# Optimization experiments

Hardware: AMD Instinct MI355X
Metric: run time of the kernel (lower is better)

The kernel has to match this reference:

```python
import jax, jax.numpy as jnp
import numpy as np

START_ID = 1  # id of the start symbol in the vocabulary


def setup_inputs() -> dict:
    key = jax.random.key(0)
    ks = jax.random.split(key, 11)
    B, T, V, E, H, F = 64, 32, 10000, 300, 256, 4096
    s = 0.05
    return {
        "X": jax.random.normal(ks[0], (B, F), jnp.float32),
        "emb_table": jax.random.normal(ks[1], (V, E), jnp.float32),
        "fc1_w": jax.random.normal(ks[2], (H, F), jnp.float32) * s,
        "fc1_b": jax.random.normal(ks[3], (H,), jnp.float32) * s,
        "w_ih": jax.random.normal(ks[4], (4 * H, H + E), jnp.float32) * s,
        "w_hh": jax.random.normal(ks[5], (4 * H, H), jnp.float32) * s,
        "b_ih": jax.random.normal(ks[6], (4 * H,), jnp.float32) * s,
        "b_hh": jax.random.normal(ks[7], (4 * H,), jnp.float32) * s,
        "fc2_w": jax.random.normal(ks[8], (V, H), jnp.float32) * s,
        "fc2_b": jax.random.normal(ks[9], (V,), jnp.float32) * s,
        "label": jax.random.randint(ks[10], (T, B), 0, V, jnp.int64),
        "max_sentence_len": T,
    }


def reference(X, emb_table, fc1_w, fc1_b, w_ih, w_hh, b_ih, b_hh, fc2_w, fc2_b,
              label, max_sentence_len):
    T = max_sentence_len
    B = X.shape[0]
    V, H = fc2_w.shape
    E = emb_table.shape[1]

    # fc1: project image features to hidden size
    Xp = X @ fc1_w.T + fc1_b  # [B, H]

    # word embedding input per step: step 1 uses start symbol,
    # step idx>=2 uses teacher-forced embedding of label[idx-1]
    start_emb = jnp.broadcast_to(emb_table[START_ID], (1, B, E))
    tf_emb = emb_table[label[1:T - 1]]          # [T-2, B, E]
    embeds = jnp.concatenate([start_emb, tf_emb], axis=0)  # [T-1, B, E]

    h0 = jnp.zeros((B, H), X.dtype)
    c0 = jnp.zeros((B, H), X.dtype)

    def step(carry, e):
        h, c = carry
        x = jnp.concatenate([Xp, e], axis=1)  # [B, H+E]
        gates = x @ w_ih.T + b_ih + h @ w_hh.T + b_hh  # [B, 4H]
        i, f, g, o = jnp.split(gates, 4, axis=1)
        i = jax.nn.sigmoid(i)
        f = jax.nn.sigmoid(f)
        g = jnp.tanh(g)
        o = jax.nn.sigmoid(o)
        c = f * c + i * g
        h = o * jnp.tanh(c)
        logp = jax.nn.log_softmax(h @ fc2_w.T + fc2_b, axis=-1)  # [B, V]
        return (h, c), logp

    _, probs = jax.lax.scan(step, (h0, c0), embeds)  # [T-1, B, V]

    # first timestep: one-hot of the start word (as in the torch code)
    start_onehot = jnp.zeros((1, B, V), X.dtype).at[:, :, START_ID].set(1.0)
    result = jnp.concatenate([start_onehot, probs], axis=0)  # [T, B, V]
    return jnp.transpose(result, (1, 0, 2))  # [B, T, V]
```

## Files before the change

kernel.cpp:

```cpp
#include <hip/hip_runtime.h>
#include <hip/hip_bf16.h>
#include <math.h>

#define B_   64
#define T_   32
#define S_   31
#define V_   10000
#define E_   300
#define H_   256
#define F_   4096
#define G4   1024
#define HE   556
#define MPAD 2048
#define NPAD 10112
#define START_ID 1
#define NBL  4

typedef __bf16 bf16x8 __attribute__((ext_vector_type(8)));
typedef float  f32x4  __attribute__((ext_vector_type(4)));

__device__ __forceinline__ float bf16bits_to_f(unsigned int u) {
    union { unsigned int i; float f; } c; c.i = u; return c.f;
}
__device__ __forceinline__ unsigned short f_to_bf16bits(float f) {
    union { float f; unsigned int i; } c; c.f = f;
    unsigned int r = c.i + 0x7fffu + ((c.i >> 16) & 1);
    return (unsigned short)(r >> 16);
}
__device__ __forceinline__ float sigm(float x) { return 1.f / (1.f + __expf(-x)); }
__device__ __forceinline__ float tanh_fast(float x) { return 1.f - 2.f / (__expf(2.f * x) + 1.f); }

__global__ void k_prep(const float* __restrict__ fc2_w,
                       __hip_bfloat16* __restrict__ fc2bf,
                       __hip_bfloat16* __restrict__ Hs,
                       float* __restrict__ Xp) {
    size_t i = (size_t)blockIdx.x * 256 + threadIdx.x;
    float v = (i < (size_t)V_ * H_) ? fc2_w[i] : 0.f;
    fc2bf[i] = __float2bfloat16(v);
    if (i < (size_t)(MPAD - S_ * B_) * H_)
        Hs[(size_t)S_ * B_ * H_ + i] = __float2bfloat16(0.f);
    if (i < B_ * H_) Xp[i] = 0.f;
}

__global__ void k_wpack(const float* __restrict__ w_hh, unsigned short* __restrict__ wpack) {
    int tid = blockIdx.x * 256 + threadIdx.x;
    int lane = tid & 63, frag = tid >> 6;
    int kf = frag & 7, nt = (frag >> 3) & 7, w = frag >> 6;
    int l16 = lane & 15, quad = lane >> 4;
    int j = (l16 & 3) * 256 + w * 32 + nt * 4 + (l16 >> 2);
    int k0 = kf * 32 + quad * 8;
    const float* src = w_hh + (size_t)j * H_ + k0;
    float4 a0 = *(const float4*)(src);
    float4 a1 = *(const float4*)(src + 4);
    unsigned short pk[8];
    pk[0] = f_to_bf16bits(a0.x); pk[1] = f_to_bf16bits(a0.y);
    pk[2] = f_to_bf16bits(a0.z); pk[3] = f_to_bf16bits(a0.w);
    pk[4] = f_to_bf16bits(a1.x); pk[5] = f_to_bf16bits(a1.y);
    pk[6] = f_to_bf16bits(a1.z); pk[7] = f_to_bf16bits(a1.w);
    uint4 st;
    st.x = (unsigned)pk[0] | ((unsigned)pk[1] << 16);
    st.y = (unsigned)pk[2] | ((unsigned)pk[3] << 16);
    st.z = (unsigned)pk[4] | ((unsigned)pk[5] << 16);
    st.w = (unsigned)pk[6] | ((unsigned)pk[7] << 16);
    *(uint4*)(wpack + (size_t)frag * 512 + lane * 8) = st;
}

__global__ void k_onehot(float* __restrict__ out) {
    int i = blockIdx.x * 256 + threadIdx.x;
    if (i < B_ * V_) {
        int b = i / V_, v = i - b * V_;
        out[(size_t)b * T_ * V_ + v] = (v == START_ID) ? 1.f : 0.f;
    }
}

__global__ void k_xp(const float* __restrict__ X, const float* __restrict__ fc1_w,
                     const float* __restrict__ fc1_b, float* __restrict__ Xp) {
    __shared__ __align__(16) float xs[1024];
    int b = blockIdx.x, q = blockIdx.y;
    const float4* xrow = (const float4*)(X + (size_t)b * F_ + q * 1024);
    if (threadIdx.x < 256) ((float4*)xs)[threadIdx.x] = xrow[threadIdx.x];
    __syncthreads();
    int k = threadIdx.x;
    const float4* w = (const float4*)(fc1_w + (size_t)k * F_ + q * 1024);
    float acc = 0.f;
    #pragma unroll 8
    for (int f = 0; f < 256; ++f) {
        float4 wv = w[f];
        float4 xv = ((const float4*)xs)[f];
        acc += wv.x * xv.x + wv.y * xv.y + wv.z * xv.z + wv.w * xv.w;
    }
    if (q == 0) acc += fc1_b[k];
    atomicAdd(&Xp[b * H_ + k], acc);
}

__global__ void k_gconst(const float* __restrict__ Xp, const float* __restrict__ w_ih,
                         const float* __restrict__ b_ih, const float* __restrict__ b_hh,
                         float* __restrict__ gconst) {
    __shared__ __align__(16) float xs[H_];
    int b = blockIdx.x;
    xs[threadIdx.x] = Xp[b * H_ + threadIdx.x];
    __syncthreads();
    #pragma unroll
    for (int q = 0; q < 4; ++q) {
        int j = threadIdx.x + q * 256;
        const float* w = w_ih + (size_t)j * HE;
        float acc = 0.f;
        #pragma unroll 8
        for (int k = 0; k < H_ / 4; ++k) {
            float4 wv = *(const float4*)(w + k * 4);
            float4 xv = ((const float4*)xs)[k];
            acc += wv.x * xv.x + wv.y * xv.y + wv.z * xv.z + wv.w * xv.w;
        }
        gconst[b * G4 + j] = acc + b_ih[j] + b_hh[j];
    }
}

__global__ void k_ge(const float* __restrict__ emb, const int* __restrict__ label,
                     const float* __restrict__ w_ih, const float* __restrict__ gconst,
                     unsigned short* __restrict__ gfullT) {
    __shared__ __align__(16) float es[8][E_];
    int jt = blockIdx.x, bt = blockIdx.y, t = blockIdx.z;
    for (int i = threadIdx.x; i < 8 * E_; i += 256) {
        int b8 = i / E_, e = i - b8 * E_;
        int b = bt * 8 + b8;
        int idx = (t == 0) ? START_ID : label[t * B_ + b];
        es[b8][e] = emb[(size_t)idx * E_ + e];
    }
    __syncthreads();
    int j = jt * 256 + threadIdx.x;
    const float* w = w_ih + (size_t)j * HE + H_;
    float acc[8] = {0.f, 0.f, 0.f, 0.f, 0.f, 0.f, 0.f, 0.f};
    for (int kk = 0; kk < E_ / 4; ++kk) {
        float4 wv = *(const float4*)(w + kk * 4);
        #pragma unroll
        for (int b8 = 0; b8 < 8; ++b8) {
            float4 ev = *(const float4*)(&es[b8][kk * 4]);
            acc[b8] += wv.x * ev.x + wv.y * ev.y + wv.z * ev.z + wv.w * ev.w;
        }
    }
    int u = threadIdx.x;
    int tile = u >> 2;
    int m = (u & 3) * 4 + jt;
    size_t base = ((((size_t)t * NBL + (bt >> 1)) * 64 + tile) * 16 + (bt & 1) * 8) * 16 + m;
    #pragma unroll
    for (int b8 = 0; b8 < 8; ++b8)
        gfullT[base + (size_t)b8 * 16] =
            f_to_bf16bits(acc[b8] + gconst[(bt * 8 + b8) * G4 + j]);
}

__global__ __launch_bounds__(512, 2) void k_lstm(const unsigned short* __restrict__ gfullT,
                                                 const unsigned short* __restrict__ wpack,
                                                 __hip_bfloat16* __restrict__ Hs_) {
    unsigned short* Hs = (unsigned short*)Hs_;
    int bg = blockIdx.x;
    int tid = threadIdx.x;
    int w = tid >> 6, lane = tid & 63;
    int l16 = lane & 15, quad = lane >> 4;

    __shared__ __align__(16) unsigned short hs[16 * 264];
    __shared__ __align__(16) unsigned short blds[8 * 16 * 64 * 8];

    const unsigned short* wpb = wpack + (size_t)(w * 8) * 8 * 512 + lane * 8;
    bf16x8 wr0[8], wr1[8];
    #pragma unroll
    for (int kf = 0; kf < 8; ++kf) wr0[kf] = *(const bf16x8*)(wpb + (0 * 8 + kf) * 512);
    #pragma unroll
    for (int kf = 0; kf < 8; ++kf) wr1[kf] = *(const bf16x8*)(wpb + (1 * 8 + kf) * 512);

    #pragma unroll
    for (int f2 = 0; f2 < 16; ++f2) {
        int nt = 2 + (f2 >> 3), kf = f2 & 7;
        bf16x8 v = *(const bf16x8*)(wpb + (nt * 8 + kf) * 512);
        *(bf16x8*)(blds + ((size_t)(w * 16 + f2) * 64 + lane) * 8) = v;
    }

    for (int i = tid; i < 16 * 264 / 8; i += 512)
        ((uint4*)hs)[i] = make_uint4(0, 0, 0, 0);
    __syncthreads();

    float c[8] = {0.f, 0.f, 0.f, 0.f, 0.f, 0.f, 0.f, 0.f};
    const unsigned short* bl = blds + (size_t)(w * 16) * 512 + lane * 8;
    const unsigned short* hb = hs + l16 * 264 + quad * 8;
    int orow = tid >> 5, ocol = tid & 31;

    for (int t = 0; t < S_; ++t) {
        if (t > 0) {
            uint4 v = *(const uint4*)(hs + orow * 264 + ocol * 8);
            *(uint4*)(Hs + ((size_t)((t - 1) * B_ + bg * 16 + orow)) * H_ + ocol * 8) = v;
        }
        uint2 gf[8];
        const unsigned short* gtb = gfullT +
            ((((size_t)t * NBL + bg) * 64 + w * 8) * 256) + l16 * 16 + quad * 4;
        #pragma unroll
        for (int nt = 0; nt < 8; ++nt) gf[nt] = *(const uint2*)(gtb + nt * 256);
        bf16x8 hf[8];
        #pragma unroll
        for (int kf = 0; kf < 8; ++kf) hf[kf] = *(const bf16x8*)(hb + kf * 32);
        __syncthreads();

        bf16x8 s4[8], s5[8];
        #pragma unroll
        for (int kf = 0; kf < 8; ++kf) s4[kf] = *(const bf16x8*)(wpb + (4 * 8 + kf) * 512);
        #pragma unroll
        for (int kf = 0; kf < 8; ++kf) s5[kf] = *(const bf16x8*)(wpb + (5 * 8 + kf) * 512);

#define DO_NT(nt, WSRC)                                                         \
        {                                                                       \
            f32x4 acc;                                                          \
            acc[0] = bf16bits_to_f(gf[nt].x << 16);                             \
            acc[1] = bf16bits_to_f(gf[nt].x & 0xffff0000u);                     \
            acc[2] = bf16bits_to_f(gf[nt].y << 16);                             \
            acc[3] = bf16bits_to_f(gf[nt].y & 0xffff0000u);                     \
            _Pragma("unroll")                                                   \
            for (int kf = 0; kf < 8; ++kf)                                      \
                acc = __builtin_amdgcn_mfma_f32_16x16x32_bf16(WSRC[kf], hf[kf], \
                                                              acc, 0, 0, 0);   \
            float ig = sigm(acc[0]);                                            \
            float fg = sigm(acc[1]);                                            \
            float gg = tanh_fast(acc[2]);                                       \
            float og = sigm(acc[3]);                                            \
            c[nt] = fg * c[nt] + ig * gg;                                       \
            float hv = og * tanh_fast(c[nt]);                                   \
            hs[l16 * 264 + w * 32 + (nt) * 4 + quad] = f_to_bf16bits(hv);       \
        }

        DO_NT(0, wr0)
        DO_NT(1, wr1)
        {
            bf16x8 w2[8];
            #pragma unroll
            for (int kf = 0; kf < 8; ++kf) w2[kf] = *(const bf16x8*)(bl + kf * 512);
            DO_NT(2, w2)
        }
        {
            bf16x8 w3[8];
            #pragma unroll
            for (int kf = 0; kf < 8; ++kf) w3[kf] = *(const bf16x8*)(bl + (8 + kf) * 512);
            DO_NT(3, w3)
        }
        bf16x8 s6[8];
        #pragma unroll
        for (int kf = 0; kf < 8; ++kf) s6[kf] = *(const bf16x8*)(wpb + (6 * 8 + kf) * 512);
        DO_NT(4, s4)
        bf16x8 s7[8];
        #pragma unroll
        for (int kf = 0; kf < 8; ++kf) s7[kf] = *(const bf16x8*)(wpb + (7 * 8 + kf) * 512);
        DO_NT(5, s5)
        DO_NT(6, s6)
        DO_NT(7, s7)
#undef DO_NT
        __syncthreads();
    }
    {
        uint4 v = *(const uint4*)(hs + orow * 264 + ocol * 8);
        *(uint4*)(Hs + ((size_t)((S_ - 1) * B_ + bg * 16 + orow)) * H_ + ocol * 8) = v;
    }
}

__global__ __launch_bounds__(256) void k_gemm(const unsigned short* __restrict__ A,
                                              const unsigned short* __restrict__ Bw,
                                              const float* __restrict__ bias,
                                              float* __restrict__ out) {
    int nt = blockIdx.x, mt = blockIdx.y;
    int w = threadIdx.x >> 6, lane = threadIdx.x & 63;
    int l16 = lane & 15, quad = lane >> 4;
    int m0 = mt * 128 + (w >> 1) * 64;
    int n0 = nt * 128 + (w & 1) * 64;
    f32x4 acc[4][4] = {};
    const unsigned short* Ap = A + (size_t)(m0 + l16) * H_ + quad * 8;
    const unsigned short* Bp = Bw + (size_t)(n0 + l16) * H_ + quad * 8;
    #pragma unroll
    for (int k = 0; k < H_; k += 32) {
        bf16x8 a[4], bb[4];
        #pragma unroll
        for (int i = 0; i < 4; ++i) {
            a[i]  = *(const bf16x8*)(Ap + (size_t)i * 16 * H_ + k);
            bb[i] = *(const bf16x8*)(Bp + (size_t)i * 16 * H_ + k);
        }
        #pragma unroll
        for (int i = 0; i < 4; ++i)
            #pragma unroll
            for (int jn = 0; jn < 4; ++jn)
                acc[i][jn] = __builtin_amdgcn_mfma_f32_16x16x32_bf16(a[i], bb[jn], acc[i][jn], 0, 0, 0);
    }
    #pragma unroll
    for (int i = 0; i < 4; ++i) {
        #pragma unroll
        for (int jn = 0; jn < 4; ++jn) {
            #pragma unroll
            for (int r = 0; r < 4; ++r) {
                int m = m0 + i * 16 + quad * 4 + r;
                int n = n0 + jn * 16 + l16;
                if (m < S_ * B_ && n < V_) {
                    int t = m >> 6, b = m & 63;
                    out[((size_t)b * T_ + t + 1) * V_ + n] = acc[i][jn][r] + bias[n];
                }
            }
        }
    }
}

__global__ void k_lsm(float* __restrict__ out) {
    __shared__ float rmx[256], rsum[256];
    int m = blockIdx.x;
    int t = m >> 6, b = m & 63;
    float* row = out + ((size_t)b * T_ + t + 1) * V_;
    int tid = threadIdx.x;
    float mx = -1e30f, sum = 0.f;
    for (int v4 = tid; v4 < V_ / 4; v4 += 256) {
        float4 x = ((const float4*)row)[v4];
        float m4 = fmaxf(fmaxf(x.x, x.y), fmaxf(x.z, x.w));
        if (m4 > mx) { sum *= __expf(mx - m4); mx = m4; }
        sum += __expf(x.x - mx) + __expf(x.y - mx) + __expf(x.z - mx) + __expf(x.w - mx);
    }
    rmx[tid] = mx; rsum[tid] = sum;
    __syncthreads();
    for (int s = 128; s > 0; s >>= 1) {
        if (tid < s) {
            float ma = rmx[tid], mb = rmx[tid + s];
            float sa = rsum[tid], sb = rsum[tid + s];
            float mm = fmaxf(ma, mb);
            rmx[tid] = mm;
            rsum[tid] = sa * __expf(ma - mm) + sb * __expf(mb - mm);
        }
        __syncthreads();
    }
    float lse = rmx[0] + logf(rsum[0]);
    for (int v4 = tid; v4 < V_ / 4; v4 += 256) {
        float4 x = ((const float4*)row)[v4];
        x.x -= lse; x.y -= lse; x.z -= lse; x.w -= lse;
        ((float4*)row)[v4] = x;
    }
}

extern "C" void kernel_launch(void* const* d_in, const int* in_sizes, int n_in,
                              void* d_out, int out_size, void* d_ws, size_t ws_size,
                              hipStream_t stream) {
    const float* X      = (const float*)d_in[0];
    const float* emb    = (const float*)d_in[1];
    const float* fc1_w  = (const float*)d_in[2];
    const float* fc1_b  = (const float*)d_in[3];
    const float* w_ih   = (const float*)d_in[4];
    const float* w_hh   = (const float*)d_in[5];
    const float* b_ih   = (const float*)d_in[6];
    const float* b_hh   = (const float*)d_in[7];
    const float* fc2_w  = (const float*)d_in[8];
    const float* fc2_b  = (const float*)d_in[9];
    const int*   label  = (const int*)d_in[10];
    float* out = (float*)d_out;

    char* ws = (char*)d_ws;
    float*          Xp     = (float*)(ws);
    float*          gconst = (float*)(ws + 65536);
    unsigned short* gfullT = (unsigned short*)(ws + 327680);
    __hip_bfloat16* Hs     = (__hip_bfloat16*)(ws + 4390912);
    __hip_bfloat16* fc2bf  = (__hip_bfloat16*)(ws + 5439488);
    unsigned short* wpack  = (unsigned short*)(ws + 10616832);

    k_prep  <<<NPAD, 256, 0, stream>>>(fc2_w, fc2bf, Hs, Xp);
    k_wpack <<<128, 256, 0, stream>>>(w_hh, wpack);
    k_onehot<<<(B_ * V_ + 255) / 256, 256, 0, stream>>>(out);
    k_xp    <<<dim3(B_, 4), 256, 0, stream>>>(X, fc1_w, fc1_b, Xp);
    k_gconst<<<B_, 256, 0, stream>>>(Xp, w_ih, b_ih, b_hh, gconst);
    k_ge    <<<dim3(4, 8, S_), 256, 0, stream>>>(emb, label, w_ih, gconst, gfullT);
    k_lstm  <<<NBL, 512, 0, stream>>>(gfullT, wpack, Hs);
    k_gemm  <<<dim3(NPAD / 128, MPAD / 128), 256, 0, stream>>>((const unsigned short*)Hs,
                                                              (const unsigned short*)fc2bf, fc2_b, out);
    k_lsm   <<<S_ * B_, 256, 0, stream>>>(out);
}
```

Baseline: 477.8 us.

## Fuse front-end kernels, transpose w_ih embedding slice, keep more LSTM weights in registers

Result: no change. 473.4 us (-0.9%).

```diff
diff --git a/kernel.cpp b/kernel.cpp
--- a/kernel.cpp
+++ b/kernel.cpp
@@ -16,6 +16,12 @@
 #define START_ID 1
 #define NBL  4
 
+#define FP0 10112
+#define FP1 (FP0 + 128)
+#define FP2 (FP1 + 2500)
+#define FP3 (FP2 + 512)
+#define FP4 (FP3 + 300)
+
 typedef __bf16 bf16x8 __attribute__((ext_vector_type(8)));
 typedef float  f32x4  __attribute__((ext_vector_type(4)));
 
@@ -30,75 +36,87 @@
 __device__ __forceinline__ float sigm(float x) { return 1.f / (1.f + __expf(-x)); }
 __device__ __forceinline__ float tanh_fast(float x) { return 1.f - 2.f / (__expf(2.f * x) + 1.f); }
 
-__global__ void k_prep(const float* __restrict__ fc2_w,
-                       __hip_bfloat16* __restrict__ fc2bf,
-                       __hip_bfloat16* __restrict__ Hs,
-                       float* __restrict__ Xp) {
-    size_t i = (size_t)blockIdx.x * 256 + threadIdx.x;
-    float v = (i < (size_t)V_ * H_) ? fc2_w[i] : 0.f;
-    fc2bf[i] = __float2bfloat16(v);
-    if (i < (size_t)(MPAD - S_ * B_) * H_)
-        Hs[(size_t)S_ * B_ * H_ + i] = __float2bfloat16(0.f);
-    if (i < B_ * H_) Xp[i] = 0.f;
-}
-
-__global__ void k_wpack(const float* __restrict__ w_hh, unsigned short* __restrict__ wpack) {
-    int tid = blockIdx.x * 256 + threadIdx.x;
-    int lane = tid & 63, frag = tid >> 6;
-    int kf = frag & 7, nt = (frag >> 3) & 7, w = frag >> 6;
-    int l16 = lane & 15, quad = lane >> 4;
-    int j = (l16 & 3) * 256 + w * 32 + nt * 4 + (l16 >> 2);
-    int k0 = kf * 32 + quad * 8;
-    const float* src = w_hh + (size_t)j * H_ + k0;
-    float4 a0 = *(const float4*)(src);
-    float4 a1 = *(const float4*)(src + 4);
-    unsigned short pk[8];
-    pk[0] = f_to_bf16bits(a0.x); pk[1] = f_to_bf16bits(a0.y);
-    pk[2] = f_to_bf16bits(a0.z); pk[3] = f_to_bf16bits(a0.w);
-    pk[4] = f_to_bf16bits(a1.x); pk[5] = f_to_bf16bits(a1.y);
-    pk[6] = f_to_bf16bits(a1.z); pk[7] = f_to_bf16bits(a1.w);
-    uint4 st;
-    st.x = (unsigned)pk[0] | ((unsigned)pk[1] << 16);
-    st.y = (unsigned)pk[2] | ((unsigned)pk[3] << 16);
-    st.z = (unsigned)pk[4] | ((unsigned)pk[5] << 16);
-    st.w = (unsigned)pk[6] | ((unsigned)pk[7] << 16);
-    *(uint4*)(wpack + (size_t)frag * 512 + lane * 8) = st;
-}
-
-__global__ void k_onehot(float* __restrict__ out) {
-    int i = blockIdx.x * 256 + threadIdx.x;
-    if (i < B_ * V_) {
-        int b = i / V_, v = i - b * V_;
-        out[(size_t)b * T_ * V_ + v] = (v == START_ID) ? 1.f : 0.f;
-    }
-}
-
-__global__ void k_xp(const float* __restrict__ X, const float* __restrict__ fc1_w,
-                     const float* __restrict__ fc1_b, float* __restrict__ Xp) {
-    __shared__ __align__(16) float xs[1024];
-    int b = blockIdx.x, q = blockIdx.y;
-    const float4* xrow = (const float4*)(X + (size_t)b * F_ + q * 1024);
-    if (threadIdx.x < 256) ((float4*)xs)[threadIdx.x] = xrow[threadIdx.x];
-    __syncthreads();
-    int k = threadIdx.x;
-    const float4* w = (const float4*)(fc1_w + (size_t)k * F_ + q * 1024);
-    float acc = 0.f;
-    #pragma unroll 8
-    for (int f = 0; f < 256; ++f) {
-        float4 wv = w[f];
-        float4 xv = ((const float4*)xs)[f];
-        acc += wv.x * xv.x + wv.y * xv.y + wv.z * xv.z + wv.w * xv.w;
-    }
-    if (q == 0) acc += fc1_b[k];
-    atomicAdd(&Xp[b * H_ + k], acc);
-}
-
-__global__ void k_gconst(const float* __restrict__ Xp, const float* __restrict__ w_ih,
+__global__ void k_front(const float* __restrict__ fc2_w,
+                        __hip_bfloat16* __restrict__ fc2bf,
+                        __hip_bfloat16* __restrict__ Hs,
+                        const float* __restrict__ w_hh,
+                        unsigned short* __restrict__ wpack,
+                        float* __restrict__ out,
+                        const float* __restrict__ X,
+                        const float* __restrict__ fc1_w,
+                        const float* __restrict__ fc1_b,
+                        float* __restrict__ Xp_part,
+                        const float* __restrict__ w_ih,
+                        float* __restrict__ wie) {
+    int bid = blockIdx.x, tid = threadIdx.x;
+    if (bid < FP0) {
+        size_t i = (size_t)bid * 256 + tid;
+        float v = (i < (size_t)V_ * H_) ? fc2_w[i] : 0.f;
+        fc2bf[i] = __float2bfloat16(v);
+        if (i < (size_t)(MPAD - S_ * B_) * H_)
+            Hs[(size_t)S_ * B_ * H_ + i] = __float2bfloat16(0.f);
+    } else if (bid < FP1) {
+        int t = (bid - FP0) * 256 + tid;
+        int lane = t & 63, frag = t >> 6;
+        int kf = frag & 7, nt = (frag >> 3) & 7, w = frag >> 6;
+        int l16 = lane & 15, quad = lane >> 4;
+        int j = (l16 & 3) * 256 + w * 32 + nt * 4 + (l16 >> 2);
+        int k0 = kf * 32 + quad * 8;
+        const float* src = w_hh + (size_t)j * H_ + k0;
+        float4 a0 = *(const float4*)(src);
+        float4 a1 = *(const float4*)(src + 4);
+        unsigned short pk[8];
+        pk[0] = f_to_bf16bits(a0.x); pk[1] = f_to_bf16bits(a0.y);
+        pk[2] = f_to_bf16bits(a0.z); pk[3] = f_to_bf16bits(a0.w);
+        pk[4] = f_to_bf16bits(a1.x); pk[5] = f_to_bf16bits(a1.y);
+        pk[6] = f_to_bf16bits(a1.z); pk[7] = f_to_bf16bits(a1.w);
+        uint4 st;
+        st.x = (unsigned)pk[0] | ((unsigned)pk[1] << 16);
+        st.y = (unsigned)pk[2] | ((unsigned)pk[3] << 16);
+        st.z = (unsigned)pk[4] | ((unsigned)pk[5] << 16);
+        st.w = (unsigned)pk[6] | ((unsigned)pk[7] << 16);
+        *(uint4*)(wpack + (size_t)frag * 512 + lane * 8) = st;
+    } else if (bid < FP2) {
+        int i = (bid - FP1) * 256 + tid;
+        if (i < B_ * V_) {
+            int b = i / V_, v = i - b * V_;
+            out[(size_t)b * T_ * V_ + v] = (v == START_ID) ? 1.f : 0.f;
+        }
+    } else if (bid < FP3) {
+        __shared__ __align__(16) float xs[512];
+        int r = bid - FP2;
+        int b = r >> 3, q = r & 7;
+        const float4* xrow = (const float4*)(X + (size_t)b * F_ + q * 512);
+        if (tid < 128) ((float4*)xs)[tid] = xrow[tid];
+        __syncthreads();
+        int k = tid;
+        const float4* w = (const float4*)(fc1_w + (size_t)k * F_ + q * 512);
+        float acc = 0.f;
+        #pragma unroll 8
+        for (int f = 0; f < 128; ++f) {
+            float4 wv = w[f];
+            float4 xv = ((const float4*)xs)[f];
+            acc += wv.x * xv.x + wv.y * xv.y + wv.z * xv.z + wv.w * xv.w;
+        }
+        if (q == 0) acc += fc1_b[k];
+        Xp_part[((size_t)(q * 64 + b)) * 256 + k] = acc;
+    } else if (bid < FP4) {
+        int idx = (bid - FP3) * 256 + tid;
+        int kk = idx >> 10, j = idx & 1023;
+        float4 v = *(const float4*)(w_ih + (size_t)j * HE + H_ + kk * 4);
+        ((float4*)wie)[(size_t)kk * 1024 + j] = v;
+    }
+}
+
+__global__ void k_gconst(const float* __restrict__ Xp_part, const float* __restrict__ w_ih,
                          const float* __restrict__ b_ih, const float* __restrict__ b_hh,
                          float* __restrict__ gconst) {
     __shared__ __align__(16) float xs[H_];
     int b = blockIdx.x;
-    xs[threadIdx.x] = Xp[b * H_ + threadIdx.x];
+    float s = 0.f;
+    #pragma unroll
+    for (int q = 0; q < 8; ++q) s += Xp_part[((size_t)(q * 64 + b)) * 256 + threadIdx.x];
+    xs[threadIdx.x] = s;
     __syncthreads();
     #pragma unroll
     for (int q = 0; q < 4; ++q) {
@@ -116,7 +134,7 @@
 }
 
 __global__ void k_ge(const float* __restrict__ emb, const int* __restrict__ label,
-                     const float* __restrict__ w_ih, const float* __restrict__ gconst,
+                     const float* __restrict__ wie, const float* __restrict__ gconst,
                      unsigned short* __restrict__ gfullT) {
     __shared__ __align__(16) float es[8][E_];
     int jt = blockIdx.x, bt = blockIdx.y, t = blockIdx.z;
@@ -128,10 +146,10 @@
     }
     __syncthreads();
     int j = jt * 256 + threadIdx.x;
-    const float* w = w_ih + (size_t)j * HE + H_;
+    const float4* wp4 = (const float4*)wie + j;
     float acc[8] = {0.f, 0.f, 0.f, 0.f, 0.f, 0.f, 0.f, 0.f};
     for (int kk = 0; kk < E_ / 4; ++kk) {
-        float4 wv = *(const float4*)(w + kk * 4);
+        float4 wv = wp4[(size_t)kk * 1024];
         #pragma unroll
         for (int b8 = 0; b8 < 8; ++b8) {
             float4 ev = *(const float4*)(&es[b8][kk * 4]);
@@ -148,9 +166,11 @@
             f_to_bf16bits(acc[b8] + gconst[(bt * 8 + b8) * G4 + j]);
 }
 
-__global__ __launch_bounds__(512, 2) void k_lstm(const unsigned short* __restrict__ gfullT,
-                                                 const unsigned short* __restrict__ wpack,
-                                                 __hip_bfloat16* __restrict__ Hs_) {
+__global__ __launch_bounds__(512)
+__attribute__((amdgpu_waves_per_eu(2, 2)))
+void k_lstm(const unsigned short* __restrict__ gfullT,
+            const unsigned short* __restrict__ wpack,
+            __hip_bfloat16* __restrict__ Hs_) {
     unsigned short* Hs = (unsigned short*)Hs_;
     int bg = blockIdx.x;
     int tid = threadIdx.x;
@@ -161,15 +181,19 @@
     __shared__ __align__(16) unsigned short blds[8 * 16 * 64 * 8];
 
     const unsigned short* wpb = wpack + (size_t)(w * 8) * 8 * 512 + lane * 8;
-    bf16x8 wr0[8], wr1[8];
+    bf16x8 wr0[8], wr1[8], wr2[8], wr3[8];
     #pragma unroll
     for (int kf = 0; kf < 8; ++kf) wr0[kf] = *(const bf16x8*)(wpb + (0 * 8 + kf) * 512);
     #pragma unroll
     for (int kf = 0; kf < 8; ++kf) wr1[kf] = *(const bf16x8*)(wpb + (1 * 8 + kf) * 512);
+    #pragma unroll
+    for (int kf = 0; kf < 8; ++kf) wr2[kf] = *(const bf16x8*)(wpb + (2 * 8 + kf) * 512);
+    #pragma unroll
+    for (int kf = 0; kf < 8; ++kf) wr3[kf] = *(const bf16x8*)(wpb + (3 * 8 + kf) * 512);
 
     #pragma unroll
     for (int f2 = 0; f2 < 16; ++f2) {
-        int nt = 2 + (f2 >> 3), kf = f2 & 7;
+        int nt = 4 + (f2 >> 3), kf = f2 & 7;
         bf16x8 v = *(const bf16x8*)(wpb + (nt * 8 + kf) * 512);
         *(bf16x8*)(blds + ((size_t)(w * 16 + f2) * 64 + lane) * 8) = v;
     }
@@ -185,8 +209,8 @@
 
     for (int t = 0; t < S_; ++t) {
         if (t > 0) {
-            uint4 v = *(const uint4*)(hs + orow * 264 + ocol * 8);
-            *(uint4*)(Hs + ((size_t)((t - 1) * B_ + bg * 16 + orow)) * H_ + ocol * 8) = v;
+            uint4 wv = *(const uint4*)(hs + orow * 264 + ocol * 8);
+            *(uint4*)(Hs + ((size_t)((t - 1) * B_ + bg * 16 + orow)) * H_ + ocol * 8) = wv;
         }
         uint2 gf[8];
         const unsigned short* gtb = gfullT +
@@ -198,11 +222,9 @@
         for (int kf = 0; kf < 8; ++kf) hf[kf] = *(const bf16x8*)(hb + kf * 32);
         __syncthreads();
 
-        bf16x8 s4[8], s5[8];
-        #pragma unroll
-        for (int kf = 0; kf < 8; ++kf) s4[kf] = *(const bf16x8*)(wpb + (4 * 8 + kf) * 512);
-        #pragma unroll
-        for (int kf = 0; kf < 8; ++kf) s5[kf] = *(const bf16x8*)(wpb + (5 * 8 + kf) * 512);
+        bf16x8 s6[8];
+        #pragma unroll
+        for (int kf = 0; kf < 8; ++kf) s6[kf] = *(const bf16x8*)(wpb + (6 * 8 + kf) * 512);
 
 #define DO_NT(nt, WSRC)                                                         \
         {                                                                       \
@@ -226,26 +248,23 @@
 
         DO_NT(0, wr0)
         DO_NT(1, wr1)
+        DO_NT(2, wr2)
+        DO_NT(3, wr3)
         {
-            bf16x8 w2[8];
+            bf16x8 w4[8];
             #pragma unroll
-            for (int kf = 0; kf < 8; ++kf) w2[kf] = *(const bf16x8*)(bl + kf * 512);
-            DO_NT(2, w2)
-        }
+            for (int kf = 0; kf < 8; ++kf) w4[kf] = *(const bf16x8*)(bl + kf * 512);
+            DO_NT(4, w4)
+        }
+        bf16x8 s7[8];
+        #pragma unroll
+        for (int kf = 0; kf < 8; ++kf) s7[kf] = *(const bf16x8*)(wpb + (7 * 8 + kf) * 512);
         {
-            bf16x8 w3[8];
+            bf16x8 w5[8];
             #pragma unroll
-            for (int kf = 0; kf < 8; ++kf) w3[kf] = *(const bf16x8*)(bl + (8 + kf) * 512);
-            DO_NT(3, w3)
-        }
-        bf16x8 s6[8];
-        #pragma unroll
-        for (int kf = 0; kf < 8; ++kf) s6[kf] = *(const bf16x8*)(wpb + (6 * 8 + kf) * 512);
-        DO_NT(4, s4)
-        bf16x8 s7[8];
-        #pragma unroll
-        for (int kf = 0; kf < 8; ++kf) s7[kf] = *(const bf16x8*)(wpb + (7 * 8 + kf) * 512);
-        DO_NT(5, s5)
+            for (int kf = 0; kf < 8; ++kf) w5[kf] = *(const bf16x8*)(bl + (8 + kf) * 512);
+            DO_NT(5, w5)
+        }
         DO_NT(6, s6)
         DO_NT(7, s7)
 #undef DO_NT
@@ -300,7 +319,8 @@
     }
 }
 
-__global__ void k_lsm(float* __restrict__ out) {
+__global__ __launch_bounds__(256) void k_lsm(float* __restrict__ out) {
+    __shared__ __align__(16) float rowbuf[V_];
     __shared__ float rmx[256], rsum[256];
     int m = blockIdx.x;
     int t = m >> 6, b = m & 63;
@@ -309,6 +329,7 @@
     float mx = -1e30f, sum = 0.f;
     for (int v4 = tid; v4 < V_ / 4; v4 += 256) {
         float4 x = ((const float4*)row)[v4];
+        ((float4*)rowbuf)[v4] = x;
         float m4 = fmaxf(fmaxf(x.x, x.y), fmaxf(x.z, x.w));
         if (m4 > mx) { sum *= __expf(mx - m4); mx = m4; }
         sum += __expf(x.x - mx) + __expf(x.y - mx) + __expf(x.z - mx) + __expf(x.w - mx);
@@ -327,7 +348,7 @@
     }
     float lse = rmx[0] + logf(rsum[0]);
     for (int v4 = tid; v4 < V_ / 4; v4 += 256) {
-        float4 x = ((const float4*)row)[v4];
+        float4 x = ((const float4*)rowbuf)[v4];
         x.x -= lse; x.y -= lse; x.z -= lse; x.w -= lse;
         ((float4*)row)[v4] = x;
     }
@@ -350,19 +371,18 @@
     float* out = (float*)d_out;
 
     char* ws = (char*)d_ws;
-    float*          Xp     = (float*)(ws);
-    float*          gconst = (float*)(ws + 65536);
-    unsigned short* gfullT = (unsigned short*)(ws + 327680);
-    __hip_bfloat16* Hs     = (__hip_bfloat16*)(ws + 4390912);
-    __hip_bfloat16* fc2bf  = (__hip_bfloat16*)(ws + 5439488);
-    unsigned short* wpack  = (unsigned short*)(ws + 10616832);
-
-    k_prep  <<<NPAD, 256, 0, stream>>>(fc2_w, fc2bf, Hs, Xp);
-    k_wpack <<<128, 256, 0, stream>>>(w_hh, wpack);
-    k_onehot<<<(B_ * V_ + 255) / 256, 256, 0, stream>>>(out);
-    k_xp    <<<dim3(B_, 4), 256, 0, stream>>>(X, fc1_w, fc1_b, Xp);
-    k_gconst<<<B_, 256, 0, stream>>>(Xp, w_ih, b_ih, b_hh, gconst);
-    k_ge    <<<dim3(4, 8, S_), 256, 0, stream>>>(emb, label, w_ih, gconst, gfullT);
+    float*          Xp_part = (float*)(ws);
+    float*          gconst  = (float*)(ws + 524288);
+    unsigned short* gfullT  = (unsigned short*)(ws + 786432);
+    __hip_bfloat16* Hs      = (__hip_bfloat16*)(ws + 4849664);
+    __hip_bfloat16* fc2bf   = (__hip_bfloat16*)(ws + 5898240);
+    unsigned short* wpack   = (unsigned short*)(ws + 11075584);
+    float*          wie     = (float*)(ws + 11599872);
+
+    k_front <<<FP4, 256, 0, stream>>>(fc2_w, fc2bf, Hs, w_hh, wpack, out,
+                                      X, fc1_w, fc1_b, Xp_part, w_ih, wie);
+    k_gconst<<<B_, 256, 0, stream>>>(Xp_part, w_ih, b_ih, b_hh, gconst);
+    k_ge    <<<dim3(4, 8, S_), 256, 0, stream>>>(emb, label, wie, gconst, gfullT);
     k_lstm  <<<NBL, 512, 0, stream>>>(gfullT, wpack, Hs);
     k_gemm  <<<dim3(NPAD / 128, MPAD / 128), 256, 0, stream>>>((const unsigned short*)Hs,
                                                               (const unsigned short*)fc2bf, fc2_b, out);
```
